# Performance work log

Hardware: AMD Instinct MI355X
Metric: run time of the kernel (lower is better)

The kernel has to match this reference:

```python
import jax, jax.numpy as jnp
import numpy as np
from jax import lax

H = 2048      # d_inner
N = 8         # half of d_state (conjugate-pair complex modes)
B, L, D_MODEL = 4, 4096, 1024
D_CONV = 4


def setup_inputs() -> dict:
    key = jax.random.key(0)
    ks = jax.random.split(key, 10)
    hidden_states = jax.random.normal(ks[0], (B, L, D_MODEL), dtype=jnp.float32)
    W_in = jax.random.normal(ks[1], (2 * H, D_MODEL), dtype=jnp.float32) / np.sqrt(D_MODEL)
    conv_w = jax.random.normal(ks[2], (H, D_CONV), dtype=jnp.float32) / np.sqrt(D_CONV)
    conv_b = jax.random.normal(ks[3], (H,), dtype=jnp.float32) * 0.1
    # S4D params: dt ~ loguniform(1e-3, 1e-1); A = -0.5 + i*pi*n (legs-ish diag init)
    u = jax.random.uniform(ks[4], (H,), dtype=jnp.float32)
    log_dt = jnp.log(1e-3) + u * (jnp.log(1e-1) - jnp.log(1e-3))
    log_A_real = jnp.log(0.5 * jnp.ones((H, N), dtype=jnp.float32))
    A_imag = jnp.pi * jnp.broadcast_to(jnp.arange(N, dtype=jnp.float32), (H, N)).copy()
    C_re = jax.random.normal(ks[5], (H, N), dtype=jnp.float32)
    C_im = jax.random.normal(ks[6], (H, N), dtype=jnp.float32)
    D = jnp.ones((H,), dtype=jnp.float32)
    W_out = jax.random.normal(ks[7], (D_MODEL, H), dtype=jnp.float32) / np.sqrt(H)
    return dict(hidden_states=hidden_states, W_in=W_in, conv_w=conv_w, conv_b=conv_b,
                log_dt=log_dt, log_A_real=log_A_real, A_imag=A_imag,
                C_re=C_re, C_im=C_im, D=D, W_out=W_out)


def _s4d_kernel(log_dt, log_A_real, A_imag, C_re, C_im, L):
    # S4D (diagonal SSM) convolution kernel, ZOH-style discretization.
    dt = jnp.exp(log_dt)                       # (H,)
    A = -jnp.exp(log_A_real) + 1j * A_imag      # (H,N) complex
    C = C_re + 1j * C_im                        # (H,N)
    dtA = dt[:, None] * A                       # (H,N)
    Ct = C * (jnp.exp(dtA) - 1.0) / A           # (H,N)
    t = jnp.arange(L, dtype=jnp.float32)
    vand = jnp.exp(dtA[:, :, None] * t)         # (H,N,L) Vandermonde
    return 2.0 * jnp.einsum('hn,hnl->hl', Ct, vand).real  # (H,L)


def reference(hidden_states, W_in, conv_w, conv_b, log_dt, log_A_real, A_imag, C_re, C_im, D, W_out):
    B, L, _ = hidden_states.shape
    # in_proj (no bias): (B,L,D) -> (B, 2H, L)
    xz = jnp.einsum('bld,ed->bel', hidden_states, W_in)
    x, z = jnp.split(xz, 2, axis=1)             # each (B,H,L)
    # causal depthwise conv1d + SiLU
    w = conv_w.shape[-1]
    xp = jnp.pad(x, ((0, 0), (0, 0), (w - 1, 0)))
    x = lax.conv_general_dilated(xp, conv_w[:, None, :], (1,), 'VALID',
                                 dimension_numbers=('NCH', 'OIH', 'NCH'),
                                 feature_group_count=x.shape[1])
    x = jax.nn.silu(x + conv_b[None, :, None])
    # S4 FFT long convolution + D skip
    k = _s4d_kernel(log_dt, log_A_real, A_imag, C_re, C_im, L)  # (H,L)
    n = 2 * L
    y = jnp.fft.irfft(jnp.fft.rfft(x, n=n) * jnp.fft.rfft(k, n=n), n=n)[..., :L]
    y = y + x * D[None, :, None]
    # SiLU gate and out_proj
    y = y * jax.nn.silu(z)
    return jnp.einsum('bhl,dh->bld', y, W_out)
```

## Files before the change

### kernel.cpp

```cpp
#include <hip/hip_runtime.h>
#include <hip/hip_bf16.h>
#include <math.h>

#define H_DIM 2048
#define N_ST 8
#define B_SZ 4
#define L_SEQ 4096
#define DMODEL 1024
#define DCONV 4
#define CL 128
#define NC (L_SEQ / CL)

typedef __bf16 bf16x8 __attribute__((ext_vector_type(8)));
typedef __bf16 bf16x4 __attribute__((ext_vector_type(4)));
typedef float f32x4 __attribute__((ext_vector_type(4)));

typedef const unsigned int __attribute__((address_space(1)))* gptr_t;
typedef unsigned int __attribute__((address_space(3)))* lptr_t;

__device__ __forceinline__ void gl_lds16(const __bf16* g, __bf16* l) {
    __builtin_amdgcn_global_load_lds((gptr_t)g, (lptr_t)l, 16, 0, 0);
}

#define WS_XZ     0
#define WS_YTH    8388608
#define WS_YTL    12582912
#define WS_COEF   16777216
#define WS_STATES 16875520
#define WS_LOOK   17924096
#define WS_HF     18186240
#define WS_WIF    24477696
#define WS_WOH    30769152
#define WS_WOL    31817728

__global__ __launch_bounds__(256) void cvt_split4(const float* __restrict__ s,
                                                  __bf16* __restrict__ h,
                                                  __bf16* __restrict__ l, int n4) {
    int i = blockIdx.x * 256 + threadIdx.x;
    if (i >= n4) return;
    float4 v = ((const float4*)s)[i];
    float vv[4] = {v.x, v.y, v.z, v.w};
    bf16x4 hv, lv;
#pragma unroll
    for (int j = 0; j < 4; ++j) {
        __bf16 hb = (__bf16)vv[j];
        hv[j] = hb;
        lv[j] = (__bf16)(vv[j] - (float)hb);
    }
    *(bf16x4*)&h[(size_t)i * 4] = hv;
    *(bf16x4*)&l[(size_t)i * 4] = lv;
}

template <int BSIDE>
__global__ __launch_bounds__(256) void cvt_fuse(const float* __restrict__ s,
                                                __bf16* __restrict__ d, int nOct) {
    int i = blockIdx.x * 256 + threadIdx.x;
    if (i >= nOct) return;
    int row = i >> 7, ko = i & 127;
    const float* p = s + (size_t)row * 1024 + ko * 8;
    float4 v0 = *(const float4*)p;
    float4 v1 = *(const float4*)(p + 4);
    float vv[8] = {v0.x, v0.y, v0.z, v0.w, v1.x, v1.y, v1.z, v1.w};
    bf16x8 hv, lv;
#pragma unroll
    for (int j = 0; j < 8; ++j) {
        __bf16 hb = (__bf16)vv[j];
        hv[j] = hb;
        lv[j] = (__bf16)(vv[j] - (float)hb);
    }
    __bf16* o = d + (size_t)row * 3072 + ko * 24;
    if (BSIDE) {
        *(bf16x8*)(o) = hv; *(bf16x8*)(o + 8) = lv; *(bf16x8*)(o + 16) = hv;
    } else {
        *(bf16x8*)(o) = hv; *(bf16x8*)(o + 8) = hv; *(bf16x8*)(o + 16) = lv;
    }
}

__global__ void coef_kernel(const float* __restrict__ log_dt,
                            const float* __restrict__ log_A_real,
                            const float* __restrict__ A_imag,
                            const float* __restrict__ C_re,
                            const float* __restrict__ C_im,
                            float* __restrict__ coef) {
    int i = blockIdx.x * blockDim.x + threadIdx.x;
    if (i >= H_DIM * N_ST) return;
    int h = i >> 3;
    float dt = expf(log_dt[h]);
    float Ar = -expf(log_A_real[i]);
    float Ai = A_imag[i];
    float er = expf(dt * Ar);
    float ang = dt * Ai;
    float wr = er * cosf(ang);
    float wi = er * sinf(ang);
    float den = Ar * Ar + Ai * Ai;
    float qr = ((wr - 1.f) * Ar + wi * Ai) / den;
    float qi = (wi * Ar - (wr - 1.f) * Ai) / den;
    float Cr = C_re[i], Ci = C_im[i];
    float Ctr = Cr * qr - Ci * qi;
    float Cti = Cr * qi + Ci * qr;
    float eCL = expf((float)CL * dt * Ar);
    float aCL = (float)CL * dt * Ai;
    float pr = eCL * cosf(aCL);
    float pi = eCL * sinf(aCL);
    const int HN = H_DIM * N_ST;
    coef[i]          = wr;
    coef[HN + i]     = wi;
    coef[2 * HN + i] = Ctr;
    coef[3 * HN + i] = Cti;
    coef[4 * HN + i] = pr;
    coef[5 * HN + i] = pi;
}

__global__ __launch_bounds__(512, 2) void gemm_f256p(const __bf16* __restrict__ A,
                                                     const __bf16* __restrict__ B,
                                                     float* __restrict__ C,
                                                     int K, int ldc) {
    __shared__ __bf16 sA[32768], sB[32768];
    const int tid = threadIdx.x;
    const int lane = tid & 63;
    const int wid = tid >> 6;
    const int wrw = wid >> 2, wcw = wid & 3;
    const int bm = blockIdx.y, bn = blockIdx.x;

    f32x4 acc[8][4];
#pragma unroll
    for (int m = 0; m < 8; ++m)
#pragma unroll
        for (int n = 0; n < 4; ++n) acc[m][n] = (f32x4){0.f, 0.f, 0.f, 0.f};

    const int kb = lane >> 4, rr = lane & 15;

    const int f0 = tid, f1 = 512 + tid;
    const int kA0 = f0 >> 8, rA0 = f0 & 255;
    const int kA1 = f1 >> 8, rA1 = f1 & 255;
    const size_t gA0 = (size_t)(bm * 256 + rA0) * K;
    const size_t gA1 = (size_t)(bm * 256 + rA1) * K;
    const size_t gB0 = (size_t)(bn * 256 + rA0) * K;
    const size_t gB1 = (size_t)(bn * 256 + rA1) * K;
    const int dst0 = kA0 * 2048 + rA0 * 8;
    const int dst1 = kA1 * 2048 + rA1 * 8;

    auto stageA = [&](int t, int ks) {
        const int base = (t & 1) * 16384 + ks * 8192;
        const size_t go = (size_t)t * 64 + ks * 32;
        gl_lds16(A + gA0 + go + kA0 * 8, &sA[base + dst0]);
        gl_lds16(A + gA1 + go + kA1 * 8, &sA[base + dst1]);
    };
    auto stageB = [&](int t, int ks) {
        const int base = (t & 1) * 16384 + ks * 8192;
        const size_t go = (size_t)t * 64 + ks * 32;
        gl_lds16(B + gB0 + go + kA0 * 8, &sB[base + dst0]);
        gl_lds16(B + gB1 + go + kA1 * 8, &sB[base + dst1]);
    };

    const int nt = K >> 6;
    stageA(0, 0); stageB(0, 0); stageA(0, 1); stageB(0, 1);
    asm volatile("s_waitcnt vmcnt(0)" ::: "memory");
    __builtin_amdgcn_s_barrier();
    __builtin_amdgcn_sched_barrier(0);

#pragma unroll 1
    for (int t = 0; t < nt; ++t) {
        const int par = (t & 1) * 16384;
        const bool pf = (t + 1 < nt);
        bf16x8 fB[4], fA[4];

        {
            const int bA = par, bB = par;
#pragma unroll
            for (int n = 0; n < 4; ++n)
                fB[n] = *(const bf16x8*)&sB[bB + kb * 2048 + (wcw * 64 + n * 16 + rr) * 8];
#pragma unroll
            for (int m = 0; m < 4; ++m)
                fA[m] = *(const bf16x8*)&sA[bA + kb * 2048 + (wrw * 128 + m * 16 + rr) * 8];
            if (pf) stageA(t + 1, 0);
            __builtin_amdgcn_s_barrier();
            asm volatile("s_waitcnt lgkmcnt(0)" ::: "memory");
            __builtin_amdgcn_sched_barrier(0);
            __builtin_amdgcn_s_setprio(1);
#pragma unroll
            for (int m = 0; m < 4; ++m)
#pragma unroll
                for (int n = 0; n < 4; ++n)
                    acc[m][n] = __builtin_amdgcn_mfma_f32_16x16x32_bf16(fA[m], fB[n], acc[m][n], 0, 0, 0);
            __builtin_amdgcn_s_setprio(0);
            __builtin_amdgcn_s_barrier();
            __builtin_amdgcn_sched_barrier(0);
        }
        {
            const int bA = par;
#pragma unroll
            for (int m = 0; m < 4; ++m)
                fA[m] = *(const bf16x8*)&sA[bA + kb * 2048 + (wrw * 128 + 64 + m * 16 + rr) * 8];
            if (pf) stageB(t + 1, 0);
            __builtin_amdgcn_s_barrier();
            asm volatile("s_waitcnt lgkmcnt(0)" ::: "memory");
            __builtin_amdgcn_sched_barrier(0);
            __builtin_amdgcn_s_setprio(1);
#pragma unroll
            for (int m = 0; m < 4; ++m)
#pragma unroll
                for (int n = 0; n < 4; ++n)
                    acc[4 + m][n] = __builtin_amdgcn_mfma_f32_16x16x32_bf16(fA[m], fB[n], acc[4 + m][n], 0, 0, 0);
            __builtin_amdgcn_s_setprio(0);
            if (pf) asm volatile("s_waitcnt vmcnt(4)" ::: "memory");
            else    asm volatile("s_waitcnt vmcnt(0)" ::: "memory");
            __builtin_amdgcn_s_barrier();
            __builtin_amdgcn_sched_barrier(0);
        }
        {
            const int bA = par + 8192, bB = par + 8192;
#pragma unroll
            for (int n = 0; n < 4; ++n)
                fB[n] = *(const bf16x8*)&sB[bB + kb * 2048 + (wcw * 64 + n * 16 + rr) * 8];
#pragma unroll
            for (int m = 0; m < 4; ++m)
                fA[m] = *(const bf16x8*)&sA[bA + kb * 2048 + (wrw * 128 + m * 16 + rr) * 8];
            if (pf) stageA(t + 1, 1);
            __builtin_amdgcn_s_barrier();
            asm volatile("s_waitcnt lgkmcnt(0)" ::: "memory");
            __builtin_amdgcn_sched_barrier(0);
            __builtin_amdgcn_s_setprio(1);
#pragma unroll
            for (int m = 0; m < 4; ++m)
#pragma unroll
                for (int n = 0; n < 4; ++n)
                    acc[m][n] = __builtin_amdgcn_mfma_f32_16x16x32_bf16(fA[m], fB[n], acc[m][n], 0, 0, 0);
            __builtin_amdgcn_s_setprio(0);
            __builtin_amdgcn_s_barrier();
            __builtin_amdgcn_sched_barrier(0);
        }
        {
            const int bA = par + 8192;
#pragma unroll
            for (int m = 0; m < 4; ++m)
                fA[m] = *(const bf16x8*)&sA[bA + kb * 2048 + (wrw * 128 + 64 + m * 16 + rr) * 8];
            if (pf) stageB(t + 1, 1);
            __builtin_amdgcn_s_barrier();
            asm volatile("s_waitcnt lgkmcnt(0)" ::: "memory");
            __builtin_amdgcn_sched_barrier(0);
            __builtin_amdgcn_s_setprio(1);
#pragma unroll
            for (int m = 0; m < 4; ++m)
#pragma unroll
                for (int n = 0; n < 4; ++n)
                    acc[4 + m][n] = __builtin_amdgcn_mfma_f32_16x16x32_bf16(fA[m], fB[n], acc[4 + m][n], 0, 0, 0);
            __builtin_amdgcn_s_setprio(0);
            if (pf) asm volatile("s_waitcnt vmcnt(4)" ::: "memory");
            else    asm volatile("s_waitcnt vmcnt(0)" ::: "memory");
            __builtin_amdgcn_s_barrier();
            __builtin_amdgcn_sched_barrier(0);
        }
    }

    const int rq = lane >> 4;
#pragma unroll
    for (int m = 0; m < 8; ++m)
#pragma unroll
        for (int n = 0; n < 4; ++n) {
            int col = bn * 256 + wcw * 64 + n * 16 + rr;
            int row0 = bm * 256 + wrw * 128 + m * 16 + rq * 4;
#pragma unroll
            for (int j = 0; j < 4; ++j)
                C[(size_t)(row0 + j) * ldc + col] = acc[m][n][j];
        }
}

__global__ __launch_bounds__(256, 1) void gemm_s128p(const __bf16* __restrict__ Ah,
                                                     const __bf16* __restrict__ Al,
                                                     const __bf16* __restrict__ Bh,
                                                     const __bf16* __restrict__ Bl,
                                                     float* __restrict__ C,
                                                     int K, int ldc) {
    __shared__ __bf16 sAh[2][2][4096], sAl[2][2][4096];
    __shared__ __bf16 sBh[2][2][4096], sBl[2][2][4096];
    const int tid = threadIdx.x;
    const int lane = tid & 63;
    const int wid = tid >> 6;
    const int wrw = wid >> 1, wcw = wid & 1;
    const int bm = blockIdx.y, bn = blockIdx.x;

    f32x4 acc[4][4];
#pragma unroll
    for (int m = 0; m < 4; ++m)
#pragma unroll
        for (int n = 0; n < 4; ++n) acc[m][n] = (f32x4){0.f, 0.f, 0.f, 0.f};

    const int kb = lane >> 4, rr = lane & 15;

    const int fl0 = tid, fl1 = 256 + tid;
    const int kbs0 = fl0 >> 7, rw0 = fl0 & 127;
    const int kbs1 = fl1 >> 7, rw1 = fl1 & 127;
    const size_t gAr0 = (size_t)(bm * 128 + rw0) * K;
    const size_t gAr1 = (size_t)(bm * 128 + rw1) * K;
    const size_t gBr0 = (size_t)(bn * 128 + rw0) * K;
    const size_t gBr1 = (size_t)(bn * 128 + rw1) * K;
    const int d0 = kbs0 * 1024 + rw0 * 8;
    const int d1 = kbs1 * 1024 + rw1 * 8;

    auto stA = [&](int t, int ks) {
        const int par = t & 1;
        const size_t go = (size_t)t * 64 + ks * 32;
        gl_lds16(Ah + gAr0 + go + kbs0 * 8, &sAh[par][ks][d0]);
        gl_lds16(Ah + gAr1 + go + kbs1 * 8, &sAh[par][ks][d1]);
        gl_lds16(Al + gAr0 + go + kbs0 * 8, &sAl[par][ks][d0]);
        gl_lds16(Al + gAr1 + go + kbs1 * 8, &sAl[par][ks][d1]);
    };
    auto stB = [&](int t, int ks) {
        const int par = t & 1;
        const size_t go = (size_t)t * 64 + ks * 32;
        gl_lds16(Bh + gBr0 + go + kbs0 * 8, &sBh[par][ks][d0]);
        gl_lds16(Bh + gBr1 + go + kbs1 * 8, &sBh[par][ks][d1]);
        gl_lds16(Bl + gBr0 + go + kbs0 * 8, &sBl[par][ks][d0]);
        gl_lds16(Bl + gBr1 + go + kbs1 * 8, &sBl[par][ks][d1]);
    };

    const int nt = K >> 6;
    stA(0, 0); stB(0, 0); stA(0, 1); stB(0, 1);
    asm volatile("s_waitcnt vmcnt(0)" ::: "memory");
    __builtin_amdgcn_s_barrier();
    __builtin_amdgcn_sched_barrier(0);

    bf16x8 fAh[4], fAl[4], fBh[4], fBl[4];

#pragma unroll 1
    for (int t = 0; t < nt; ++t) {
        const int par = t & 1;
        const bool pf = (t + 1 < nt);

        {
#pragma unroll
            for (int n = 0; n < 4; ++n) {
                const int off = kb * 1024 + (wcw * 64 + n * 16 + rr) * 8;
                fBh[n] = *(const bf16x8*)&sBh[par][0][off];
                fBl[n] = *(const bf16x8*)&sBl[par][0][off];
            }
#pragma unroll
            for (int m = 0; m < 4; ++m) {
                const int off = kb * 1024 + (wrw * 64 + m * 16 + rr) * 8;
                fAh[m] = *(const bf16x8*)&sAh[par][0][off];
                fAl[m] = *(const bf16x8*)&sAl[par][0][off];
            }
            if (pf) stA(t + 1, 0);
            __builtin_amdgcn_s_barrier();
            asm volatile("s_waitcnt lgkmcnt(0)" ::: "memory");
            __builtin_amdgcn_sched_barrier(0);
            __builtin_amdgcn_s_setprio(1);
#pragma unroll
            for (int m = 0; m < 2; ++m)
#pragma unroll
                for (int n = 0; n < 4; ++n) {
                    acc[m][n] = __builtin_amdgcn_mfma_f32_16x16x32_bf16(fAh[m], fBh[n], acc[m][n], 0, 0, 0);
                    acc[m][n] = __builtin_amdgcn_mfma_f32_16x16x32_bf16(fAh[m], fBl[n], acc[m][n], 0, 0, 0);
                    acc[m][n] = __builtin_amdgcn_mfma_f32_16x16x32_bf16(fAl[m], fBh[n], acc[m][n], 0, 0, 0);
                }
            __builtin_amdgcn_s_setprio(0);
            __builtin_amdgcn_s_barrier();
            __builtin_amdgcn_sched_barrier(0);
        }
        {
            if (pf) stB(t + 1, 0);
            __builtin_amdgcn_s_barrier();
            __builtin_amdgcn_sched_barrier(0);
            __builtin_amdgcn_s_setprio(1);
#pragma unroll
            for (int m = 2; m < 4; ++m)
#pragma unroll
                for (int n = 0; n < 4; ++n) {
                    acc[m][n] = __builtin_amdgcn_mfma_f32_16x16x32_bf16(fAh[m], fBh[n], acc[m][n], 0, 0, 0);
                    acc[m][n] = __builtin_amdgcn_mfma_f32_16x16x32_bf16(fAh[m], fBl[n], acc[m][n], 0, 0, 0);
                    acc[m][n] = __builtin_amdgcn_mfma_f32_16x16x32_bf16(fAl[m], fBh[n], acc[m][n], 0, 0, 0);
                }
            __builtin_amdgcn_s_setprio(0);
            if (pf) asm volatile("s_waitcnt vmcnt(8)" ::: "memory");
            else    asm volatile("s_waitcnt vmcnt(0)" ::: "memory");
            __builtin_amdgcn_s_barrier();
            __builtin_amdgcn_sched_barrier(0);
        }
        {
#pragma unroll
            for (int n = 0; n < 4; ++n) {
                const int off = kb * 1024 + (wcw * 64 + n * 16 + rr) * 8;
                fBh[n] = *(const bf16x8*)&sBh[par][1][off];
                fBl[n] = *(const bf16x8*)&sBl[par][1][off];
            }
#pragma unroll
            for (int m = 0; m < 4; ++m) {
                const int off = kb * 1024 + (wrw * 64 + m * 16 + rr) * 8;
                fAh[m] = *(const bf16x8*)&sAh[par][1][off];
                fAl[m] = *(const bf16x8*)&sAl[par][1][off];
            }
            if (pf) stA(t + 1, 1);
            __builtin_amdgcn_s_barrier();
            asm volatile("s_waitcnt lgkmcnt(0)" ::: "memory");
            __builtin_amdgcn_sched_barrier(0);
            __builtin_amdgcn_s_setprio(1);
#pragma unroll
            for (int m = 0; m < 2; ++m)
#pragma unroll
                for (int n = 0; n < 4; ++n) {
                    acc[m][n] = __builtin_amdgcn_mfma_f32_16x16x32_bf16(fAh[m], fBh[n], acc[m][n], 0, 0, 0);
                    acc[m][n] = __builtin_amdgcn_mfma_f32_16x16x32_bf16(fAh[m], fBl[n], acc[m][n], 0, 0, 0);
                    acc[m][n] = __builtin_amdgcn_mfma_f32_16x16x32_bf16(fAl[m], fBh[n], acc[m][n], 0, 0, 0);
                }
            __builtin_amdgcn_s_setprio(0);
            __builtin_amdgcn_s_barrier();
            __builtin_amdgcn_sched_barrier(0);
        }
        {
            if (pf) stB(t + 1, 1);
            __builtin_amdgcn_s_barrier();
            __builtin_amdgcn_sched_barrier(0);
            __builtin_amdgcn_s_setprio(1);
#pragma unroll
            for (int m = 2; m < 4; ++m)
#pragma unroll
                for (int n = 0; n < 4; ++n) {
                    acc[m][n] = __builtin_amdgcn_mfma_f32_16x16x32_bf16(fAh[m], fBh[n], acc[m][n], 0, 0, 0);
                    acc[m][n] = __builtin_amdgcn_mfma_f32_16x16x32_bf16(fAh[m], fBl[n], acc[m][n], 0, 0, 0);
                    acc[m][n] = __builtin_amdgcn_mfma_f32_16x16x32_bf16(fAl[m], fBh[n], acc[m][n], 0, 0, 0);
                }
            __builtin_amdgcn_s_setprio(0);
            if (pf) asm volatile("s_waitcnt vmcnt(8)" ::: "memory");
            else    asm volatile("s_waitcnt vmcnt(0)" ::: "memory");
            __builtin_amdgcn_s_barrier();
            __builtin_amdgcn_sched_barrier(0);
        }
    }

    const int rq = lane >> 4;
#pragma unroll
    for (int m = 0; m < 4; ++m)
#pragma unroll
        for (int n = 0; n < 4; ++n) {
            int col = bn * 128 + wcw * 64 + n * 16 + rr;
            int row0 = bm * 128 + wrw * 64 + m * 16 + rq * 4;
#pragma unroll
            for (int j = 0; j < 4; ++j)
                C[(size_t)(row0 + j) * ldc + col] = acc[m][n][j];
        }
}

__global__ __launch_bounds__(256) void scan_phase1(const float* __restrict__ xz,
                                                   const float* __restrict__ coef,
                                                   const float* __restrict__ conv_w,
                                                   const float* __restrict__ conv_b,
                                                   float* __restrict__ states,
                                                   float* __restrict__ look) {
    int t = blockIdx.x * 256 + threadIdx.x;
    int c = t & (NC - 1);
    int h = t >> 5;

    const int HN = H_DIM * N_ST;
    float wr[N_ST], wi[N_ST];
#pragma unroll
    for (int n = 0; n < N_ST; ++n) {
        wr[n] = coef[h * N_ST + n];
        wi[n] = coef[HN + h * N_ST + n];
    }
    float cw0 = conv_w[h * 4 + 0], cw1 = conv_w[h * 4 + 1];
    float cw2 = conv_w[h * 4 + 2], cw3 = conv_w[h * 4 + 3];
    float cb = conv_b[h];

    const float* xrow = xz + (size_t)h * L_SEQ + c * CL;
    float x3 = 0.f, x2 = 0.f, x1 = 0.f;
    if (c > 0) {
        float4 p = *(const float4*)(xrow - 4);
        x3 = p.y; x2 = p.z; x1 = p.w;
    }
    *(float4*)(look + (size_t)t * 4) = make_float4(x3, x2, x1, 0.f);

    float sr[N_ST], si[N_ST];
#pragma unroll
    for (int n = 0; n < N_ST; ++n) { sr[n] = 0.f; si[n] = 0.f; }

    for (int j = 0; j < CL; j += 4) {
        float4 v = *(const float4*)(xrow + j);
        float xv[4] = {v.x, v.y, v.z, v.w};
#pragma unroll
        for (int k = 0; k < 4; ++k) {
            float u = cw0 * x3 + cw1 * x2 + cw2 * x1 + cw3 * xv[k] + cb;
            float xc = u / (1.f + __expf(-u));
            x3 = x2; x2 = x1; x1 = xv[k];
#pragma unroll
            for (int n = 0; n < N_ST; ++n) {
                float nr = wr[n] * sr[n] - wi[n] * si[n] + xc;
                float ni = wr[n] * si[n] + wi[n] * sr[n];
                sr[n] = nr; si[n] = ni;
            }
        }
    }
    float* st = states + (size_t)t * (N_ST * 2);
#pragma unroll
    for (int n = 0; n < N_ST; ++n) { st[2 * n] = sr[n]; st[2 * n + 1] = si[n]; }
}

__global__ __launch_bounds__(256) void scan_phase2(const float* __restrict__ coef,
                                                   float* __restrict__ states) {
    int h = blockIdx.x * 256 + threadIdx.x;
    if (h >= H_DIM) return;
    const int HN = H_DIM * N_ST;
    float pr[N_ST], pi[N_ST];
#pragma unroll
    for (int n = 0; n < N_ST; ++n) {
        pr[n] = coef[4 * HN + h * N_ST + n];
        pi[n] = coef[5 * HN + h * N_ST + n];
    }
    float sr[N_ST], si[N_ST];
#pragma unroll
    for (int n = 0; n < N_ST; ++n) { sr[n] = 0.f; si[n] = 0.f; }
    float* base = states + (size_t)h * NC * (N_ST * 2);
    for (int c = 0; c < NC; ++c) {
        float* st = base + c * (N_ST * 2);
#pragma unroll
        for (int n = 0; n < N_ST; ++n) {
            float lr = st[2 * n], li = st[2 * n + 1];
            st[2 * n] = sr[n]; st[2 * n + 1] = si[n];
            float nr = pr[n] * sr[n] - pi[n] * si[n] + lr;
            float ni = pr[n] * si[n] + pi[n] * sr[n] + li;
            sr[n] = nr; si[n] = ni;
        }
    }
}

__global__ __launch_bounds__(256) void scan_phase3(float* __restrict__ xz,
                                                   const float* __restrict__ coef,
                                                   const float* __restrict__ conv_w,
                                                   const float* __restrict__ conv_b,
                                                   const float* __restrict__ Dvec,
                                                   const float* __restrict__ states,
                                                   const float* __restrict__ look) {
    int t = blockIdx.x * 256 + threadIdx.x;
    int c = t & (NC - 1);
    int h = t >> 5;

    const int HN = H_DIM * N_ST;
    float wr[N_ST], wi[N_ST], Ctr[N_ST], Cti[N_ST];
#pragma unroll
    for (int n = 0; n < N_ST; ++n) {
        wr[n]  = coef[h * N_ST + n];
        wi[n]  = coef[HN + h * N_ST + n];
        Ctr[n] = coef[2 * HN + h * N_ST + n];
        Cti[n] = coef[3 * HN + h * N_ST + n];
    }
    float cw0 = conv_w[h * 4 + 0], cw1 = conv_w[h * 4 + 1];
    float cw2 = conv_w[h * 4 + 2], cw3 = conv_w[h * 4 + 3];
    float cb = conv_b[h];
    float Dh = Dvec[h];

    float* xrow = xz + (size_t)h * L_SEQ + c * CL;
    const float* zrow = xz + (size_t)(H_DIM + h) * L_SEQ + c * CL;

    float4 lk = *(const float4*)(look + (size_t)t * 4);
    float x3 = lk.x, x2 = lk.y, x1 = lk.z;

    const float* st = states + (size_t)t * (N_ST * 2);
    float sr[N_ST], si[N_ST];
#pragma unroll
    for (int n = 0; n < N_ST; ++n) { sr[n] = st[2 * n]; si[n] = st[2 * n + 1]; }

    for (int j = 0; j < CL; j += 4) {
        float4 v = *(const float4*)(xrow + j);
        float4 zv = *(const float4*)(zrow + j);
        float xv[4] = {v.x, v.y, v.z, v.w};
        float zz[4] = {zv.x, zv.y, zv.z, zv.w};
        float out[4];
#pragma unroll
        for (int k = 0; k < 4; ++k) {
            float u = cw0 * x3 + cw1 * x2 + cw2 * x1 + cw3 * xv[k] + cb;
            float xc = u / (1.f + __expf(-u));
            x3 = x2; x2 = x1; x1 = xv[k];
            float accy = 0.f;
#pragma unroll
            for (int n = 0; n < N_ST; ++n) {
                float nr = wr[n] * sr[n] - wi[n] * si[n] + xc;
                float ni = wr[n] * si[n] + wi[n] * sr[n];
                sr[n] = nr; si[n] = ni;
                accy += Ctr[n] * nr - Cti[n] * ni;
            }
            float yv = 2.f * accy + Dh * xc;
            float g = zz[k] / (1.f + __expf(-zz[k]));
            out[k] = yv * g;
        }
        *(float4*)(xrow + j) = make_float4(out[0], out[1], out[2], out[3]);
    }
}

__global__ __launch_bounds__(256) void transpose_split(const float* __restrict__ y,
                                                       __bf16* __restrict__ th,
                                                       __bf16* __restrict__ tl) {
    __shared__ float tile[64][65];
    const int l0 = blockIdx.x * 64, h0 = blockIdx.y * 64;
    const int tid = threadIdx.x;
    const int r = tid >> 4, c4 = (tid & 15) * 4;
#pragma unroll
    for (int p = 0; p < 4; ++p) {
        float4 v = *(const float4*)(y + (size_t)(h0 + r + p * 16) * L_SEQ + l0 + c4);
        tile[r + p * 16][c4 + 0] = v.x;
        tile[r + p * 16][c4 + 1] = v.y;
        tile[r + p * 16][c4 + 2] = v.z;
        tile[r + p * 16][c4 + 3] = v.w;
    }
    __syncthreads();
    const int l = tid >> 2, hb = (tid & 3) * 16;
    float vals[16];
#pragma unroll
    for (int j = 0; j < 16; ++j) vals[j] = tile[hb + j][l];
    bf16x8 hv0, hv1, lv0, lv1;
#pragma unroll
    for (int j = 0; j < 8; ++j) {
        __bf16 hbv = (__bf16)vals[j];
        hv0[j] = hbv;
        lv0[j] = (__bf16)(vals[j] - (float)hbv);
        __bf16 hbv2 = (__bf16)vals[j + 8];
        hv1[j] = hbv2;
        lv1[j] = (__bf16)(vals[j + 8] - (float)hbv2);
    }
    size_t base = (size_t)(l0 + l) * H_DIM + h0 + hb;
    *(bf16x8*)&th[base] = hv0;
    *(bf16x8*)&th[base + 8] = hv1;
    *(bf16x8*)&tl[base] = lv0;
    *(bf16x8*)&tl[base + 8] = lv1;
}

extern "C" void kernel_launch(void* const* d_in, const int* in_sizes, int n_in,
                              void* d_out, int out_size, void* d_ws, size_t ws_size,
                              hipStream_t stream) {
    const float* hid        = (const float*)d_in[0];
    const float* W_in       = (const float*)d_in[1];
    const float* conv_w     = (const float*)d_in[2];
    const float* conv_b     = (const float*)d_in[3];
    const float* log_dt     = (const float*)d_in[4];
    const float* log_A_real = (const float*)d_in[5];
    const float* A_imag     = (const float*)d_in[6];
    const float* C_re       = (const float*)d_in[7];
    const float* C_im       = (const float*)d_in[8];
    const float* Dv         = (const float*)d_in[9];
    const float* W_out      = (const float*)d_in[10];
    float* out = (float*)d_out;
    float* ws  = (float*)d_ws;

    float* xz      = ws + WS_XZ;
    __bf16* yTh    = (__bf16*)(ws + WS_YTH);
    __bf16* yTl    = (__bf16*)(ws + WS_YTL);
    float* coef    = ws + WS_COEF;
    float* states  = ws + WS_STATES;
    float* look    = ws + WS_LOOK;
    __bf16* Hf     = (__bf16*)(ws + WS_HF);
    __bf16* WiF    = (__bf16*)(ws + WS_WIF);
    __bf16* Woh    = (__bf16*)(ws + WS_WOH);
    __bf16* Wol    = (__bf16*)(ws + WS_WOL);

    coef_kernel<<<(H_DIM * N_ST + 255) / 256, 256, 0, stream>>>(
        log_dt, log_A_real, A_imag, C_re, C_im, coef);

    const int wOct = 2 * H_DIM * DMODEL / 8;
    cvt_fuse<0><<<(wOct + 255) / 256, 256, 0, stream>>>(W_in, WiF, wOct);
    cvt_split4<<<(DMODEL * H_DIM / 4 + 255) / 256, 256, 0, stream>>>(W_out, Woh, Wol, DMODEL * H_DIM / 4);

    const int nscan = H_DIM * NC;
    const int hOct = L_SEQ * DMODEL / 8;
    dim3 gIn(L_SEQ / 256, 2 * H_DIM / 256);
    dim3 gOut(DMODEL / 128, L_SEQ / 128);
    dim3 gTr(L_SEQ / 64, H_DIM / 64);

    for (int b = 0; b < B_SZ; ++b) {
        const float* hid_b = hid + (size_t)b * L_SEQ * DMODEL;
        float* out_b = out + (size_t)b * L_SEQ * DMODEL;

        cvt_fuse<1><<<(hOct + 255) / 256, 256, 0, stream>>>(hid_b, Hf, hOct);
        gemm_f256p<<<gIn, 512, 0, stream>>>(WiF, Hf, xz, 3 * DMODEL, L_SEQ);
        scan_phase1<<<nscan / 256, 256, 0, stream>>>(xz, coef, conv_w, conv_b, states, look);
        scan_phase2<<<(H_DIM + 255) / 256, 256, 0, stream>>>(coef, states);
        scan_phase3<<<nscan / 256, 256, 0, stream>>>(xz, coef, conv_w, conv_b, Dv, states, look);
        transpose_split<<<gTr, 256, 0, stream>>>(xz, yTh, yTl);
        gemm_s128p<<<gOut, 256, 0, stream>>>(yTh, yTl, Woh, Wol, out_b, H_DIM, DMODEL);
    }
}
```

Measured before the change: 1.467 ms.

## Fuse transpose and bf16 split into scan phase 3, drop lookback buffer

Scan phase 3 now writes the gated output directly as transposed hi/lo bf16 pairs, so the separate transpose_split kernel and the fp32 write-back of y into xz go away. Threads are remapped so that the 64 lanes of a wavefront cover 64 consecutive channels, which makes each per-timestep bf16 store contiguous across the wave. The conv lookback buffer is removed and both scan kernels reread the three preceding x values directly. The yTh buffer now reuses the Hf workspace region, and the trade-off is 2-byte scattered stores per timestep in place of a tiled shared-memory transpose.

```diff
diff --git a/kernel.cpp b/kernel.cpp
--- a/kernel.cpp
+++ b/kernel.cpp
@@ -23,15 +23,13 @@
 }
 
 #define WS_XZ     0
-#define WS_YTH    8388608
-#define WS_YTL    12582912
 #define WS_COEF   16777216
 #define WS_STATES 16875520
-#define WS_LOOK   17924096
-#define WS_HF     18186240
-#define WS_WIF    24477696
-#define WS_WOH    30769152
-#define WS_WOL    31817728
+#define WS_HF     17924096
+#define WS_WIF    24215552
+#define WS_WOH    30507008
+#define WS_WOL    31555584
+#define WS_YTL    32604160
 
 __global__ __launch_bounds__(256) void cvt_split4(const float* __restrict__ s,
                                                   __bf16* __restrict__ h,
@@ -445,8 +443,7 @@
                                                    const float* __restrict__ coef,
                                                    const float* __restrict__ conv_w,
                                                    const float* __restrict__ conv_b,
-                                                   float* __restrict__ states,
-                                                   float* __restrict__ look) {
+                                                   float* __restrict__ states) {
     int t = blockIdx.x * 256 + threadIdx.x;
     int c = t & (NC - 1);
     int h = t >> 5;
@@ -468,7 +465,6 @@
         float4 p = *(const float4*)(xrow - 4);
         x3 = p.y; x2 = p.z; x1 = p.w;
     }
-    *(float4*)(look + (size_t)t * 4) = make_float4(x3, x2, x1, 0.f);
 
     float sr[N_ST], si[N_ST];
 #pragma unroll
@@ -523,16 +519,19 @@
     }
 }
 
-__global__ __launch_bounds__(256) void scan_phase3(float* __restrict__ xz,
-                                                   const float* __restrict__ coef,
-                                                   const float* __restrict__ conv_w,
-                                                   const float* __restrict__ conv_b,
-                                                   const float* __restrict__ Dvec,
-                                                   const float* __restrict__ states,
-                                                   const float* __restrict__ look) {
-    int t = blockIdx.x * 256 + threadIdx.x;
-    int c = t & (NC - 1);
-    int h = t >> 5;
+__global__ __launch_bounds__(256) void scan_phase3t(const float* __restrict__ xz,
+                                                    const float* __restrict__ coef,
+                                                    const float* __restrict__ conv_w,
+                                                    const float* __restrict__ conv_b,
+                                                    const float* __restrict__ Dvec,
+                                                    const float* __restrict__ states,
+                                                    __bf16* __restrict__ th,
+                                                    __bf16* __restrict__ tl) {
+    const int lane = threadIdx.x & 63;
+    const int wv = threadIdx.x >> 6;
+    const int c = blockIdx.x * 4 + wv;
+    const int h = blockIdx.y * 64 + lane;
+    const int t = h * NC + c;
 
     const int HN = H_DIM * N_ST;
     float wr[N_ST], wi[N_ST], Ctr[N_ST], Cti[N_ST];
@@ -548,23 +547,28 @@
     float cb = conv_b[h];
     float Dh = Dvec[h];
 
-    float* xrow = xz + (size_t)h * L_SEQ + c * CL;
+    const float* xrow = xz + (size_t)h * L_SEQ + c * CL;
     const float* zrow = xz + (size_t)(H_DIM + h) * L_SEQ + c * CL;
 
-    float4 lk = *(const float4*)(look + (size_t)t * 4);
-    float x3 = lk.x, x2 = lk.y, x1 = lk.z;
+    float x3 = 0.f, x2 = 0.f, x1 = 0.f;
+    if (c > 0) {
+        float4 p = *(const float4*)(xrow - 4);
+        x3 = p.y; x2 = p.z; x1 = p.w;
+    }
 
     const float* st = states + (size_t)t * (N_ST * 2);
     float sr[N_ST], si[N_ST];
 #pragma unroll
     for (int n = 0; n < N_ST; ++n) { sr[n] = st[2 * n]; si[n] = st[2 * n + 1]; }
+
+    __bf16* thp = th + (size_t)(c * CL) * H_DIM + h;
+    __bf16* tlp = tl + (size_t)(c * CL) * H_DIM + h;
 
     for (int j = 0; j < CL; j += 4) {
         float4 v = *(const float4*)(xrow + j);
         float4 zv = *(const float4*)(zrow + j);
         float xv[4] = {v.x, v.y, v.z, v.w};
         float zz[4] = {zv.x, zv.y, zv.z, zv.w};
-        float out[4];
 #pragma unroll
         for (int k = 0; k < 4; ++k) {
             float u = cw0 * x3 + cw1 * x2 + cw2 * x1 + cw3 * xv[k] + cb;
@@ -580,47 +584,13 @@
             }
             float yv = 2.f * accy + Dh * xc;
             float g = zz[k] / (1.f + __expf(-zz[k]));
-            out[k] = yv * g;
-        }
-        *(float4*)(xrow + j) = make_float4(out[0], out[1], out[2], out[3]);
-    }
-}
-
-__global__ __launch_bounds__(256) void transpose_split(const float* __restrict__ y,
-                                                       __bf16* __restrict__ th,
-                                                       __bf16* __restrict__ tl) {
-    __shared__ float tile[64][65];
-    const int l0 = blockIdx.x * 64, h0 = blockIdx.y * 64;
-    const int tid = threadIdx.x;
-    const int r = tid >> 4, c4 = (tid & 15) * 4;
-#pragma unroll
-    for (int p = 0; p < 4; ++p) {
-        float4 v = *(const float4*)(y + (size_t)(h0 + r + p * 16) * L_SEQ + l0 + c4);
-        tile[r + p * 16][c4 + 0] = v.x;
-        tile[r + p * 16][c4 + 1] = v.y;
-        tile[r + p * 16][c4 + 2] = v.z;
-        tile[r + p * 16][c4 + 3] = v.w;
-    }
-    __syncthreads();
-    const int l = tid >> 2, hb = (tid & 3) * 16;
-    float vals[16];
-#pragma unroll
-    for (int j = 0; j < 16; ++j) vals[j] = tile[hb + j][l];
-    bf16x8 hv0, hv1, lv0, lv1;
-#pragma unroll
-    for (int j = 0; j < 8; ++j) {
-        __bf16 hbv = (__bf16)vals[j];
-        hv0[j] = hbv;
-        lv0[j] = (__bf16)(vals[j] - (float)hbv);
-        __bf16 hbv2 = (__bf16)vals[j + 8];
-        hv1[j] = hbv2;
-        lv1[j] = (__bf16)(vals[j + 8] - (float)hbv2);
-    }
-    size_t base = (size_t)(l0 + l) * H_DIM + h0 + hb;
-    *(bf16x8*)&th[base] = hv0;
-    *(bf16x8*)&th[base + 8] = hv1;
-    *(bf16x8*)&tl[base] = lv0;
-    *(bf16x8*)&tl[base + 8] = lv1;
+            float val = yv * g;
+            __bf16 hb = (__bf16)val;
+            __bf16 lb = (__bf16)(val - (float)hb);
+            thp[(size_t)(j + k) * H_DIM] = hb;
+            tlp[(size_t)(j + k) * H_DIM] = lb;
+        }
+    }
 }
 
 extern "C" void kernel_launch(void* const* d_in, const int* in_sizes, int n_in,
@@ -641,15 +611,14 @@
     float* ws  = (float*)d_ws;
 
     float* xz      = ws + WS_XZ;
-    __bf16* yTh    = (__bf16*)(ws + WS_YTH);
-    __bf16* yTl    = (__bf16*)(ws + WS_YTL);
     float* coef    = ws + WS_COEF;
     float* states  = ws + WS_STATES;
-    float* look    = ws + WS_LOOK;
     __bf16* Hf     = (__bf16*)(ws + WS_HF);
     __bf16* WiF    = (__bf16*)(ws + WS_WIF);
     __bf16* Woh    = (__bf16*)(ws + WS_WOH);
     __bf16* Wol    = (__bf16*)(ws + WS_WOL);
+    __bf16* yTh    = (__bf16*)(ws + WS_HF);
+    __bf16* yTl    = (__bf16*)(ws + WS_YTL);
 
     coef_kernel<<<(H_DIM * N_ST + 255) / 256, 256, 0, stream>>>(
         log_dt, log_A_real, A_imag, C_re, C_im, coef);
@@ -662,7 +631,7 @@
     const int hOct = L_SEQ * DMODEL / 8;
     dim3 gIn(L_SEQ / 256, 2 * H_DIM / 256);
     dim3 gOut(DMODEL / 128, L_SEQ / 128);
-    dim3 gTr(L_SEQ / 64, H_DIM / 64);
+    dim3 gP3(NC / 4, H_DIM / 64);
 
     for (int b = 0; b < B_SZ; ++b) {
         const float* hid_b = hid + (size_t)b * L_SEQ * DMODEL;
@@ -670,10 +639,9 @@
 
         cvt_fuse<1><<<(hOct + 255) / 256, 256, 0, stream>>>(hid_b, Hf, hOct);
         gemm_f256p<<<gIn, 512, 0, stream>>>(WiF, Hf, xz, 3 * DMODEL, L_SEQ);
-        scan_phase1<<<nscan / 256, 256, 0, stream>>>(xz, coef, conv_w, conv_b, states, look);
+        scan_phase1<<<nscan / 256, 256, 0, stream>>>(xz, coef, conv_w, conv_b, states);
         scan_phase2<<<(H_DIM + 255) / 256, 256, 0, stream>>>(coef, states);
-        scan_phase3<<<nscan / 256, 256, 0, stream>>>(xz, coef, conv_w, conv_b, Dv, states, look);
-        transpose_split<<<gTr, 256, 0, stream>>>(xz, yTh, yTl);
+        scan_phase3t<<<gP3, 256, 0, stream>>>(xz, coef, conv_w, conv_b, Dv, states, yTh, yTl);
         gemm_s128p<<<gOut, 256, 0, stream>>>(yTh, yTl, Woh, Wol, out_b, H_DIM, DMODEL);
     }
 }
```

Result: faster. 1.424 ms (-3.0%).
